# Optimization experiments

Hardware: AMD Instinct MI355X
Metric: run time of the kernel (lower is better)

Reference implementation:

```python
import jax, jax.numpy as jnp
import numpy as np

D_M = 1024
NUM_TOK = 4096


def setup_inputs() -> dict:
    key = jax.random.key(0)
    ks = jax.random.split(key, 7)
    mk = lambda k, shp: jax.random.normal(k, shp, dtype=jnp.float32) * 0.02
    return {
        "X": jax.random.normal(ks[0], (D_M, NUM_TOK), dtype=jnp.float32),
        "W_Q": mk(ks[1], (D_M, D_M)),
        "W_K": mk(ks[2], (D_M, D_M)),
        "W_V": mk(ks[3], (D_M, D_M)),
        "W_O": mk(ks[4], (D_M, D_M)),
        "mlp_in": mk(ks[5], (D_M, D_M)),
        "mlp_out": mk(ks[6], (D_M, D_M)),
    }


def reference(X, W_Q, W_K, W_V, W_O, mlp_in, mlp_out):
    # X: [d_m, num_tok]; module transposes to tokens-major [N, d]
    Xt = X.T  # [N, d]
    N = Xt.shape[0]
    Q = Xt @ W_Q  # [N, d]
    K = Xt @ W_K  # [N, d]
    scores = Q @ K.T  # [N, N] -- NOTE: no 1/sqrt(d) scaling, as in the original
    causal = jnp.tril(jnp.ones((N, N), dtype=bool))  # keep lower triangle incl. diag
    scores = jnp.where(causal, scores, -jnp.inf)
    A = jax.nn.softmax(scores, axis=-1)  # [N, N]
    # original applies W_V then W_O to X BEFORE the attention mix
    RH = (Xt @ W_V) @ W_O  # [N, d]
    Xt = Xt + A @ RH  # residual + attention
    h = jax.nn.relu(Xt @ mlp_in)  # [N, d] (hidden dim == d_m in original)
    Xt = Xt + h @ mlp_out  # residual + MLP
    return Xt.T  # back to [d_m, num_tok]
```

## Files before the change

kernel.cpp:

```cpp
#include <hip/hip_runtime.h>
#include <stdint.h>
#include <stddef.h>

using f16 = _Float16;
typedef __attribute__((ext_vector_type(8))) _Float16 f16x8;
typedef __attribute__((ext_vector_type(4))) float f32x4;

__device__ __forceinline__ void async_copy16(const f16* g, f16* l) {
    __builtin_amdgcn_global_load_lds(
        (const __attribute__((address_space(1))) void*)g,
        (__attribute__((address_space(3))) void*)l, 16, 0, 0);
}

__global__ __launch_bounds__(256)
void prep_all(const float* __restrict__ X, float* __restrict__ Xtf,
              f16* __restrict__ Xth,
              const float* __restrict__ w0, const float* __restrict__ w1,
              const float* __restrict__ w2, const float* __restrict__ w3,
              const float* __restrict__ w4, const float* __restrict__ w5,
              f16* o0, f16* o1, f16* o2, f16* o3, f16* o4, f16* o5,
              int D, int NT) {
    __shared__ float tile[32][33];
    const int tx = threadIdx.x & 31, ty = threadIdx.x >> 5;
    int b = blockIdx.x;
    if (b < 4096) {
        const int c0 = (b & 127) * 32, r0 = (b >> 7) * 32;
#pragma unroll
        for (int j = 0; j < 4; j++)
            tile[ty + j * 8][tx] = X[(size_t)(r0 + ty + j * 8) * NT + c0 + tx];
        __syncthreads();
#pragma unroll
        for (int j = 0; j < 4; j++) {
            float v = tile[tx][ty + j * 8];
            size_t idx = (size_t)(c0 + ty + j * 8) * D + r0 + tx;
            Xtf[idx] = v;
            Xth[idx] = (f16)v;
        }
        return;
    }
    b -= 4096;
    const int z = b >> 10, r = b & 1023;
    const float* in = z == 0 ? w0 : z == 1 ? w1 : z == 2 ? w2 : z == 3 ? w3 : z == 4 ? w4 : w5;
    f16* out = z == 0 ? o0 : z == 1 ? o1 : z == 2 ? o2 : z == 3 ? o3 : z == 4 ? o4 : o5;
    const int c0 = (r & 31) * 32, r0 = (r >> 5) * 32;
    if (z < 3) {
#pragma unroll
        for (int j = 0; j < 4; j++) {
            size_t idx = (size_t)(r0 + ty + j * 8) * D + c0 + tx;
            out[idx] = (f16)in[idx];
        }
    } else {
#pragma unroll
        for (int j = 0; j < 4; j++)
            tile[ty + j * 8][tx] = in[(size_t)(r0 + ty + j * 8) * D + c0 + tx];
        __syncthreads();
#pragma unroll
        for (int j = 0; j < 4; j++)
            out[(size_t)(c0 + ty + j * 8) * D + r0 + tx] = (f16)tile[tx][ty + j * 8];
    }
}

__global__ __launch_bounds__(256)
void softmax_rows(f16* __restrict__ A, int N) {
    const int row = blockIdx.x, len = row + 1;
    const int lim = ((row >> 7) + 1) << 7;
    f16* a = A + (size_t)row * N;
    __shared__ float red[256];
    const int t = threadIdx.x;

    float v[16];
    float mx = -1e30f;
#pragma unroll
    for (int j = 0; j < 2; j++) {
        const int c = (t + j * 256) * 8;
        if (c < len) {
            f16x8 x = *(const f16x8*)(a + c);
#pragma unroll
            for (int e = 0; e < 8; e++) {
                float f = (c + e < len) ? (float)x[e] : -1e30f;
                v[j * 8 + e] = f;
                mx = fmaxf(mx, f);
            }
        } else {
#pragma unroll
            for (int e = 0; e < 8; e++) v[j * 8 + e] = -1e30f;
        }
    }
    red[t] = mx; __syncthreads();
    for (int o = 128; o > 0; o >>= 1) { if (t < o) red[t] = fmaxf(red[t], red[t + o]); __syncthreads(); }
    mx = red[0]; __syncthreads();

    float sum = 0.f;
#pragma unroll
    for (int k = 0; k < 16; k++) {
        float e = (v[k] > -1e29f) ? __expf(v[k] - mx) : 0.0f;
        v[k] = e;
        sum += e;
    }
    red[t] = sum; __syncthreads();
    for (int o = 128; o > 0; o >>= 1) { if (t < o) red[t] += red[t + o]; __syncthreads(); }
    const float inv = 1.0f / red[0];
#pragma unroll
    for (int j = 0; j < 2; j++) {
        const int c = (t + j * 256) * 8;
        if (c < lim) {
            f16x8 o8;
#pragma unroll
            for (int e = 0; e < 8; e++) o8[e] = (f16)(v[j * 8 + e] * inv);
            *(f16x8*)(a + c) = o8;
        }
    }
}


__device__ __forceinline__ void body64db(
    f16* lds, const f16* __restrict__ A, const f16* __restrict__ B,
    f16* __restrict__ Ch, int m0, int n0, int N, int K, int lda) {
    const int t = threadIdx.x;
    const int lane = t & 63, wave = t >> 6;
    const int wm = (wave >> 1) * 32, wn = (wave & 1) * 32;
    const int lm = lane & 15, lq = lane >> 4;
    const int srow = t >> 2;
    const int gs = ((t & 3) ^ ((srow >> 1) & 3)) * 8;
    const int rs = (lq ^ ((lm >> 1) & 3)) * 8;

    auto stage = [&](f16* buf, int k0) {
#pragma unroll
        for (int r = 0; r < 4; r++)
            async_copy16(A + (size_t)(m0 + srow) * lda + k0 + r * 32 + gs,
                         buf + r * 2048 + t * 8);
#pragma unroll
        for (int r = 0; r < 4; r++)
            async_copy16(B + (size_t)(n0 + srow) * K + k0 + r * 32 + gs,
                         buf + 8192 + r * 2048 + t * 8);
    };

    f32x4 acc[2][2] = {};
    stage(lds, 0);
    __syncthreads();
    int cur = 0;
    for (int k0 = 0; k0 < K; k0 += 128) {
        f16* cb = lds + cur * 16384;
        if (k0 + 128 < K) stage(lds + (cur ^ 1) * 16384, k0 + 128);
#pragma unroll
        for (int kk = 0; kk < 4; kk++) {
            f16x8 af[2], bf[2];
#pragma unroll
            for (int i = 0; i < 2; i++)
                af[i] = *(const f16x8*)&cb[kk * 2048 + (wm + i * 16 + lm) * 32 + rs];
#pragma unroll
            for (int j = 0; j < 2; j++)
                bf[j] = *(const f16x8*)&cb[8192 + kk * 2048 + (wn + j * 16 + lm) * 32 + rs];
#pragma unroll
            for (int i = 0; i < 2; i++)
#pragma unroll
                for (int j = 0; j < 2; j++)
                    acc[i][j] = __builtin_amdgcn_mfma_f32_16x16x32_f16(
                        af[i], bf[j], acc[i][j], 0, 0, 0);
        }
        __syncthreads();
        cur ^= 1;
    }

#pragma unroll
    for (int i = 0; i < 2; i++) {
        const int row = m0 + wm + i * 16 + lq * 4;
#pragma unroll
        for (int j = 0; j < 2; j++) {
            const int col = n0 + wn + j * 16 + lm;
            f32x4 v = acc[i][j];
#pragma unroll
            for (int r = 0; r < 4; r++)
                Ch[(size_t)(row + r) * N + col] = (f16)v[r];
        }
    }
}

template <int BN, int MODE>
__device__ __forceinline__ void body128db(
    f16* lds, const f16* __restrict__ A, const f16* __restrict__ B,
    float* __restrict__ Cf, f16* __restrict__ Ch, const float* __restrict__ resid,
    int m0, int n0, int M, int N, int K, int lda, int Keff) {
    const int t = threadIdx.x;
    const int lane = t & 63, wave = t >> 6;
    constexpr int WN = BN / 2;
    constexpr int NJ = WN / 16;
    constexpr int ASZ = 128 * 64;
    constexpr int BSZ = BN * 64;
    constexpr int BUF = ASZ + BSZ;
    const int wm = (wave >> 1) * 64, wn = (wave & 1) * WN;
    const int lm = lane & 15, lq = lane >> 4;
    const int srow = t >> 2;
    const int gs = ((t & 3) ^ ((srow >> 1) & 3)) * 8;
    const int rs = (lq ^ ((lm >> 1) & 3)) * 8;

    auto stage = [&](f16* buf, int k0) {
#pragma unroll
        for (int r = 0; r < 4; r++)
            async_copy16(A + (size_t)(m0 + (r & 1) * 64 + srow) * lda + k0 + (r >> 1) * 32 + gs,
                         buf + r * 2048 + t * 8);
        if constexpr (BN == 128) {
#pragma unroll
            for (int r = 0; r < 4; r++)
                async_copy16(B + (size_t)(n0 + (r & 1) * 64 + srow) * K + k0 + (r >> 1) * 32 + gs,
                             buf + ASZ + r * 2048 + t * 8);
        } else {
#pragma unroll
            for (int r = 0; r < 2; r++)
                async_copy16(B + (size_t)(n0 + srow) * K + k0 + r * 32 + gs,
                             buf + ASZ + r * 2048 + t * 8);
        }
    };

    f32x4 acc[4][NJ] = {};
    stage(lds, 0);
    __syncthreads();
    int cur = 0;
    for (int k0 = 0; k0 < Keff; k0 += 64) {
        f16* cb = lds + cur * BUF;
        if (k0 + 64 < Keff) stage(lds + (cur ^ 1) * BUF, k0 + 64);
#pragma unroll
        for (int kk = 0; kk < 2; kk++) {
            f16x8 af[4], bf[NJ];
#pragma unroll
            for (int i = 0; i < 4; i++)
                af[i] = *(const f16x8*)&cb[kk * 4096 + (wm + i * 16 + lm) * 32 + rs];
#pragma unroll
            for (int j = 0; j < NJ; j++)
                bf[j] = *(const f16x8*)&cb[ASZ + kk * (BN * 32) + (wn + j * 16 + lm) * 32 + rs];
#pragma unroll
            for (int i = 0; i < 4; i++)
#pragma unroll
                for (int j = 0; j < NJ; j++)
                    acc[i][j] = __builtin_amdgcn_mfma_f32_16x16x32_f16(
                        af[i], bf[j], acc[i][j], 0, 0, 0);
        }
        __syncthreads();
        cur ^= 1;
    }

#pragma unroll
    for (int i = 0; i < 4; i++) {
        const int row = m0 + wm + i * 16 + lq * 4;
#pragma unroll
        for (int j = 0; j < NJ; j++) {
            const int col = n0 + wn + j * 16 + lm;
            f32x4 v = acc[i][j];
#pragma unroll
            for (int r = 0; r < 4; r++) {
                if (MODE == 0) {
                    Ch[(size_t)(row + r) * N + col] = (f16)v[r];
                } else if (MODE == 2) {
                    float o = v[r] + resid[(size_t)(row + r) * N + col];
                    Cf[(size_t)(row + r) * N + col] = o;
                    Ch[(size_t)(row + r) * N + col] = (f16)o;
                } else if (MODE == 3) {
                    Ch[(size_t)(row + r) * N + col] = (f16)fmaxf(v[r], 0.0f);
                } else {
                    float o = v[r] + resid[(size_t)(row + r) * N + col];
                    Cf[(size_t)col * M + (row + r)] = o;
                }
            }
        }
    }
}

__global__ __launch_bounds__(256, 2)
void tiny_pair(const f16* Wkh, const f16* Wqh, f16* GT,
               const f16* Wot, const f16* Wvh, f16* HT) {
    __shared__ alignas(16) f16 smem[32768];
    const int b = blockIdx.x;
    if (b < 256)
        body64db(smem, Wkh, Wqh, GT,
                 (b >> 4) * 64, (b & 15) * 64, 1024, 1024, 1024);
    else {
        const int r = b - 256;
        body64db(smem, Wot, Wvh, HT,
                 (r >> 4) * 64, (r & 15) * 64, 1024, 1024, 1024);
    }
}

__global__ __launch_bounds__(256, 2)
void mid_pair(const f16* Xth, const f16* GT, f16* Qp,
              const f16* HT, f16* RHt) {
    __shared__ alignas(16) f16 smem[32768];
    const int x = blockIdx.x & 7;
    int s = blockIdx.x >> 3;
    if (s < 32) {
        const int m = x + 8 * (s >> 3), n = s & 7;
        body128db<128, 0>(smem, Xth, GT, nullptr, Qp, nullptr,
                          m * 128, n * 128, 4096, 1024, 1024, 1024, 1024);
    } else {
        s -= 32;
        const int n = x + 8 * (s >> 3), m = s & 7;
        body128db<128, 0>(smem, HT, Xth, nullptr, RHt, nullptr,
                          m * 128, n * 128, 1024, 4096, 1024, 1024, 1024);
    }
}

__global__ __launch_bounds__(256, 2)
void scores_tri(const f16* Qp, const f16* Xth, f16* Af) {
    __shared__ alignas(16) f16 smem[32768];
    const int x = blockIdx.x & 7;
    int s = blockIdx.x >> 3;
    int m = 0, n = 0;
#pragma unroll
    for (int q = 3; q >= 0; q--) {
        const int mm = 8 * q + ((q & 1) ? 7 - x : x);
        if (s < mm + 1) { m = mm; n = s; break; }
        s -= mm + 1;
    }
    body128db<128, 0>(smem, Qp, Xth, nullptr, Af, nullptr,
                      m * 128, n * 128, 4096, 4096, 1024, 1024, 1024);
}

template <int MODE, bool CAUSAL_K>
__global__ __launch_bounds__(256, 2)
void gemm_n64(const f16* __restrict__ A, const f16* __restrict__ B,
              float* __restrict__ Cf, f16* __restrict__ Ch,
              const float* __restrict__ resid, int M, int N, int K, int lda) {
    __shared__ alignas(16) f16 smem[24576];
    const int x = blockIdx.x & 7, s = blockIdx.x >> 3;
    const int qs = s >> 4, n = s & 15;
    int m;
    if (CAUSAL_K) {
        const int q = (qs == 0) ? 3 : (qs == 1) ? 2 : (qs == 2) ? 0 : 1;
        m = 8 * q + ((q & 1) ? 7 - x : x);
    } else {
        m = x + 8 * qs;
    }
    const int m0 = m * 128, n0 = n * 64;
    int Keff = K;
    if (CAUSAL_K) {
        Keff = m0 + 128;
        if (Keff > K) Keff = K;
    }
    body128db<64, MODE>(smem, A, B, Cf, Ch, resid,
                        m0, n0, M, N, K, lda, Keff);
}

extern "C" void kernel_launch(void* const* d_in, const int* in_sizes, int n_in,
                              void* d_out, int out_size, void* d_ws, size_t ws_size,
                              hipStream_t stream) {
    const int D = 1024, NT = 4096;
    const float* X = (const float*)d_in[0];
    const float* W[6] = {(const float*)d_in[1], (const float*)d_in[2],
                         (const float*)d_in[3], (const float*)d_in[4],
                         (const float*)d_in[5], (const float*)d_in[6]};
    char* ws = (char*)d_ws;
    auto MB = [](size_t x) { return x << 20; };

    float* Xtf  = (float*)(ws + MB(0));
    f16*   Xth  = (f16*)(ws + MB(16));
    f16*   Wqh  = (f16*)(ws + MB(24));
    f16*   Wkh  = (f16*)(ws + MB(26));
    f16*   Wvh  = (f16*)(ws + MB(28));
    f16*   Wot  = (f16*)(ws + MB(30));
    f16*   W4t  = (f16*)(ws + MB(32));
    f16*   W5t  = (f16*)(ws + MB(34));
    f16*   GT   = (f16*)(ws + MB(36));
    f16*   HT   = (f16*)(ws + MB(38));
    f16*   Qp   = (f16*)(ws + MB(40));
    f16*   Af   = (f16*)(ws + MB(48));
    f16*   RHt  = (f16*)(ws + MB(80));
    float* Y1f  = (float*)(ws + MB(88));
    f16*   Y1h  = (f16*)(ws + MB(104));
    f16*   hb   = (f16*)(ws + MB(40));
    float* outF = (float*)d_out;

    prep_all<<<10240, 256, 0, stream>>>(X, Xtf, Xth, W[0], W[1], W[2], W[3],
                                        W[4], W[5], Wqh, Wkh, Wvh, Wot, W4t,
                                        W5t, D, NT);

    tiny_pair<<<512, 256, 0, stream>>>(Wkh, Wqh, GT, Wot, Wvh, HT);

    mid_pair<<<512, 256, 0, stream>>>(Xth, GT, Qp, HT, RHt);

    scores_tri<<<528, 256, 0, stream>>>(Qp, Xth, Af);

    softmax_rows<<<NT, 256, 0, stream>>>(Af, NT);

    gemm_n64<2, true><<<512, 256, 0, stream>>>(
        Af, RHt, Y1f, Y1h, Xtf, NT, D, NT, NT);

    gemm_n64<3, false><<<512, 256, 0, stream>>>(
        Y1h, W4t, nullptr, hb, nullptr, NT, D, D, D);

    gemm_n64<4, false><<<512, 256, 0, stream>>>(
        hb, W5t, outF, nullptr, Y1f, NT, D, D, D);
}
```

Baseline: 241.3 us.

## Use triple-buffered 128x64 GEMM with prefetch depth two and explicit vmcnt waits

Replaces the double-buffered 128xBN GEMM body with a three-stage LDS ring that keeps two k-tiles in flight, using explicit s_waitcnt vmcnt and raw s_barrier with sched_barrier fences instead of __syncthreads. The 128x128 tiles in mid_pair and scores_tri become 128x64 tiles, doubling grid sizes and changing the triangular tile mapping. The aim is to hide global-to-LDS latency and raise wave parallelism. The cost is more LDS per block, which may limit occupancy, and the hand-counted vmcnt values must match the number of outstanding loads per stage.

```diff
diff --git a/kernel.cpp b/kernel.cpp
--- a/kernel.cpp
+++ b/kernel.cpp
@@ -10,6 +10,13 @@
     __builtin_amdgcn_global_load_lds(
         (const __attribute__((address_space(1))) void*)g,
         (__attribute__((address_space(3))) void*)l, 16, 0, 0);
+}
+
+template <int N>
+__device__ __forceinline__ void wait_vmcnt() {
+    if constexpr (N == 0)       asm volatile("s_waitcnt vmcnt(0)" ::: "memory");
+    else if constexpr (N == 6)  asm volatile("s_waitcnt vmcnt(6)" ::: "memory");
+    else if constexpr (N == 12) asm volatile("s_waitcnt vmcnt(12)" ::: "memory");
 }
 
 __global__ __launch_bounds__(256)
@@ -113,137 +120,83 @@
 }
 
 
-__device__ __forceinline__ void body64db(
+template <int MODE>
+__device__ __forceinline__ void body_pf2(
     f16* lds, const f16* __restrict__ A, const f16* __restrict__ B,
-    f16* __restrict__ Ch, int m0, int n0, int N, int K, int lda) {
+    float* __restrict__ Cf, f16* __restrict__ Ch, const float* __restrict__ resid,
+    int m0, int n0, int M, int N, int K, int lda, int Keff) {
+    constexpr int ASZ = 128 * 64;
+    constexpr int BSZ = 64 * 64;
+    constexpr int SSZ = ASZ + BSZ;
     const int t = threadIdx.x;
     const int lane = t & 63, wave = t >> 6;
-    const int wm = (wave >> 1) * 32, wn = (wave & 1) * 32;
+    const int wm = (wave >> 1) * 64, wn = (wave & 1) * 32;
     const int lm = lane & 15, lq = lane >> 4;
     const int srow = t >> 2;
     const int gs = ((t & 3) ^ ((srow >> 1) & 3)) * 8;
     const int rs = (lq ^ ((lm >> 1) & 3)) * 8;
 
+    f32x4 acc[4][2] = {};
+
     auto stage = [&](f16* buf, int k0) {
 #pragma unroll
         for (int r = 0; r < 4; r++)
-            async_copy16(A + (size_t)(m0 + srow) * lda + k0 + r * 32 + gs,
+            async_copy16(A + (size_t)(m0 + (r & 1) * 64 + srow) * lda + k0 + (r >> 1) * 32 + gs,
                          buf + r * 2048 + t * 8);
 #pragma unroll
-        for (int r = 0; r < 4; r++)
+        for (int r = 0; r < 2; r++)
             async_copy16(B + (size_t)(n0 + srow) * K + k0 + r * 32 + gs,
-                         buf + 8192 + r * 2048 + t * 8);
+                         buf + ASZ + r * 2048 + t * 8);
     };
 
-    f32x4 acc[2][2] = {};
-    stage(lds, 0);
-    __syncthreads();
-    int cur = 0;
-    for (int k0 = 0; k0 < K; k0 += 128) {
-        f16* cb = lds + cur * 16384;
-        if (k0 + 128 < K) stage(lds + (cur ^ 1) * 16384, k0 + 128);
-#pragma unroll
-        for (int kk = 0; kk < 4; kk++) {
-            f16x8 af[2], bf[2];
-#pragma unroll
-            for (int i = 0; i < 2; i++)
-                af[i] = *(const f16x8*)&cb[kk * 2048 + (wm + i * 16 + lm) * 32 + rs];
+    auto compute = [&](const f16* cb) {
+#pragma unroll
+        for (int kk = 0; kk < 2; kk++) {
+            f16x8 af[4], bf[2];
+#pragma unroll
+            for (int i = 0; i < 4; i++)
+                af[i] = *(const f16x8*)&cb[kk * 4096 + (wm + i * 16 + lm) * 32 + rs];
 #pragma unroll
             for (int j = 0; j < 2; j++)
-                bf[j] = *(const f16x8*)&cb[8192 + kk * 2048 + (wn + j * 16 + lm) * 32 + rs];
-#pragma unroll
-            for (int i = 0; i < 2; i++)
+                bf[j] = *(const f16x8*)&cb[ASZ + kk * 2048 + (wn + j * 16 + lm) * 32 + rs];
+#pragma unroll
+            for (int i = 0; i < 4; i++)
 #pragma unroll
                 for (int j = 0; j < 2; j++)
                     acc[i][j] = __builtin_amdgcn_mfma_f32_16x16x32_f16(
                         af[i], bf[j], acc[i][j], 0, 0, 0);
         }
-        __syncthreads();
-        cur ^= 1;
-    }
-
-#pragma unroll
-    for (int i = 0; i < 2; i++) {
-        const int row = m0 + wm + i * 16 + lq * 4;
-#pragma unroll
-        for (int j = 0; j < 2; j++) {
-            const int col = n0 + wn + j * 16 + lm;
-            f32x4 v = acc[i][j];
-#pragma unroll
-            for (int r = 0; r < 4; r++)
-                Ch[(size_t)(row + r) * N + col] = (f16)v[r];
-        }
-    }
-}
-
-template <int BN, int MODE>
-__device__ __forceinline__ void body128db(
-    f16* lds, const f16* __restrict__ A, const f16* __restrict__ B,
-    float* __restrict__ Cf, f16* __restrict__ Ch, const float* __restrict__ resid,
-    int m0, int n0, int M, int N, int K, int lda, int Keff) {
-    const int t = threadIdx.x;
-    const int lane = t & 63, wave = t >> 6;
-    constexpr int WN = BN / 2;
-    constexpr int NJ = WN / 16;
-    constexpr int ASZ = 128 * 64;
-    constexpr int BSZ = BN * 64;
-    constexpr int BUF = ASZ + BSZ;
-    const int wm = (wave >> 1) * 64, wn = (wave & 1) * WN;
-    const int lm = lane & 15, lq = lane >> 4;
-    const int srow = t >> 2;
-    const int gs = ((t & 3) ^ ((srow >> 1) & 3)) * 8;
-    const int rs = (lq ^ ((lm >> 1) & 3)) * 8;
-
-    auto stage = [&](f16* buf, int k0) {
-#pragma unroll
-        for (int r = 0; r < 4; r++)
-            async_copy16(A + (size_t)(m0 + (r & 1) * 64 + srow) * lda + k0 + (r >> 1) * 32 + gs,
-                         buf + r * 2048 + t * 8);
-        if constexpr (BN == 128) {
-#pragma unroll
-            for (int r = 0; r < 4; r++)
-                async_copy16(B + (size_t)(n0 + (r & 1) * 64 + srow) * K + k0 + (r >> 1) * 32 + gs,
-                             buf + ASZ + r * 2048 + t * 8);
+    };
+
+    f16 *pa = lds, *pb = lds + SSZ, *pc = lds + 2 * SSZ;
+    stage(pa, 0);
+    stage(pb, 64);
+    const int NS = Keff >> 6;
+    for (int s = 0; s < NS; s++) {
+        const int k2 = (s + 2) << 6;
+        if (k2 < Keff) {
+            stage(pc, k2);
+            wait_vmcnt<12>();
+        } else if (s + 1 < NS) {
+            wait_vmcnt<6>();
         } else {
-#pragma unroll
-            for (int r = 0; r < 2; r++)
-                async_copy16(B + (size_t)(n0 + srow) * K + k0 + r * 32 + gs,
-                             buf + ASZ + r * 2048 + t * 8);
-        }
-    };
-
-    f32x4 acc[4][NJ] = {};
-    stage(lds, 0);
-    __syncthreads();
-    int cur = 0;
-    for (int k0 = 0; k0 < Keff; k0 += 64) {
-        f16* cb = lds + cur * BUF;
-        if (k0 + 64 < Keff) stage(lds + (cur ^ 1) * BUF, k0 + 64);
-#pragma unroll
-        for (int kk = 0; kk < 2; kk++) {
-            f16x8 af[4], bf[NJ];
-#pragma unroll
-            for (int i = 0; i < 4; i++)
-                af[i] = *(const f16x8*)&cb[kk * 4096 + (wm + i * 16 + lm) * 32 + rs];
-#pragma unroll
-            for (int j = 0; j < NJ; j++)
-                bf[j] = *(const f16x8*)&cb[ASZ + kk * (BN * 32) + (wn + j * 16 + lm) * 32 + rs];
-#pragma unroll
-            for (int i = 0; i < 4; i++)
-#pragma unroll
-                for (int j = 0; j < NJ; j++)
-                    acc[i][j] = __builtin_amdgcn_mfma_f32_16x16x32_f16(
-                        af[i], bf[j], acc[i][j], 0, 0, 0);
-        }
-        __syncthreads();
-        cur ^= 1;
+            wait_vmcnt<0>();
+        }
+        __builtin_amdgcn_sched_barrier(0);
+        __builtin_amdgcn_s_barrier();
+        __builtin_amdgcn_sched_barrier(0);
+        compute(pa);
+        __builtin_amdgcn_sched_barrier(0);
+        __builtin_amdgcn_s_barrier();
+        __builtin_amdgcn_sched_barrier(0);
+        f16* tp = pa; pa = pb; pb = pc; pc = tp;
     }
 
 #pragma unroll
     for (int i = 0; i < 4; i++) {
         const int row = m0 + wm + i * 16 + lq * 4;
 #pragma unroll
-        for (int j = 0; j < NJ; j++) {
+        for (int j = 0; j < 2; j++) {
             const int col = n0 + wn + j * 16 + lm;
             f32x4 v = acc[i][j];
 #pragma unroll
@@ -265,6 +218,69 @@
     }
 }
 
+__device__ __forceinline__ void body64db(
+    f16* lds, const f16* __restrict__ A, const f16* __restrict__ B,
+    f16* __restrict__ Ch, int m0, int n0, int N, int K, int lda) {
+    const int t = threadIdx.x;
+    const int lane = t & 63, wave = t >> 6;
+    const int wm = (wave >> 1) * 32, wn = (wave & 1) * 32;
+    const int lm = lane & 15, lq = lane >> 4;
+    const int srow = t >> 2;
+    const int gs = ((t & 3) ^ ((srow >> 1) & 3)) * 8;
+    const int rs = (lq ^ ((lm >> 1) & 3)) * 8;
+
+    auto stage = [&](f16* buf, int k0) {
+#pragma unroll
+        for (int r = 0; r < 4; r++)
+            async_copy16(A + (size_t)(m0 + srow) * lda + k0 + r * 32 + gs,
+                         buf + r * 2048 + t * 8);
+#pragma unroll
+        for (int r = 0; r < 4; r++)
+            async_copy16(B + (size_t)(n0 + srow) * K + k0 + r * 32 + gs,
+                         buf + 8192 + r * 2048 + t * 8);
+    };
+
+    f32x4 acc[2][2] = {};
+    stage(lds, 0);
+    __syncthreads();
+    int cur = 0;
+    for (int k0 = 0; k0 < K; k0 += 128) {
+        f16* cb = lds + cur * 16384;
+        if (k0 + 128 < K) stage(lds + (cur ^ 1) * 16384, k0 + 128);
+#pragma unroll
+        for (int kk = 0; kk < 4; kk++) {
+            f16x8 af[2], bf[2];
+#pragma unroll
+            for (int i = 0; i < 2; i++)
+                af[i] = *(const f16x8*)&cb[kk * 2048 + (wm + i * 16 + lm) * 32 + rs];
+#pragma unroll
+            for (int j = 0; j < 2; j++)
+                bf[j] = *(const f16x8*)&cb[8192 + kk * 2048 + (wn + j * 16 + lm) * 32 + rs];
+#pragma unroll
+            for (int i = 0; i < 2; i++)
+#pragma unroll
+                for (int j = 0; j < 2; j++)
+                    acc[i][j] = __builtin_amdgcn_mfma_f32_16x16x32_f16(
+                        af[i], bf[j], acc[i][j], 0, 0, 0);
+        }
+        __syncthreads();
+        cur ^= 1;
+    }
+
+#pragma unroll
+    for (int i = 0; i < 2; i++) {
+        const int row = m0 + wm + i * 16 + lq * 4;
+#pragma unroll
+        for (int j = 0; j < 2; j++) {
+            const int col = n0 + wn + j * 16 + lm;
+            f32x4 v = acc[i][j];
+#pragma unroll
+            for (int r = 0; r < 4; r++)
+                Ch[(size_t)(row + r) * N + col] = (f16)v[r];
+        }
+    }
+}
+
 __global__ __launch_bounds__(256, 2)
 void tiny_pair(const f16* Wkh, const f16* Wqh, f16* GT,
                const f16* Wot, const f16* Wvh, f16* HT) {
@@ -283,43 +299,44 @@
 __global__ __launch_bounds__(256, 2)
 void mid_pair(const f16* Xth, const f16* GT, f16* Qp,
               const f16* HT, f16* RHt) {
-    __shared__ alignas(16) f16 smem[32768];
+    __shared__ alignas(16) f16 smem[36864];
     const int x = blockIdx.x & 7;
     int s = blockIdx.x >> 3;
-    if (s < 32) {
-        const int m = x + 8 * (s >> 3), n = s & 7;
-        body128db<128, 0>(smem, Xth, GT, nullptr, Qp, nullptr,
-                          m * 128, n * 128, 4096, 1024, 1024, 1024, 1024);
+    if (s < 64) {
+        const int m = x + 8 * (s >> 4), n = s & 15;
+        body_pf2<0>(smem, Xth, GT, nullptr, Qp, nullptr,
+                    m * 128, n * 64, 4096, 1024, 1024, 1024, 1024);
     } else {
-        s -= 32;
+        s -= 64;
         const int n = x + 8 * (s >> 3), m = s & 7;
-        body128db<128, 0>(smem, HT, Xth, nullptr, RHt, nullptr,
-                          m * 128, n * 128, 1024, 4096, 1024, 1024, 1024);
+        body_pf2<0>(smem, HT, Xth, nullptr, RHt, nullptr,
+                    m * 128, n * 64, 1024, 4096, 1024, 1024, 1024);
     }
 }
 
 __global__ __launch_bounds__(256, 2)
 void scores_tri(const f16* Qp, const f16* Xth, f16* Af) {
-    __shared__ alignas(16) f16 smem[32768];
+    __shared__ alignas(16) f16 smem[36864];
     const int x = blockIdx.x & 7;
     int s = blockIdx.x >> 3;
+    const int cand[4] = {31 - x, 16 + x, 15 - x, x};
     int m = 0, n = 0;
 #pragma unroll
-    for (int q = 3; q >= 0; q--) {
-        const int mm = 8 * q + ((q & 1) ? 7 - x : x);
-        if (s < mm + 1) { m = mm; n = s; break; }
-        s -= mm + 1;
-    }
-    body128db<128, 0>(smem, Qp, Xth, nullptr, Af, nullptr,
-                      m * 128, n * 128, 4096, 4096, 1024, 1024, 1024);
+    for (int i = 0; i < 4; i++) {
+        const int c = 2 * cand[i] + 2;
+        if (s < c) { m = cand[i]; n = s; break; }
+        s -= c;
+    }
+    body_pf2<0>(smem, Qp, Xth, nullptr, Af, nullptr,
+                m * 128, n * 64, 4096, 4096, 1024, 1024, 1024);
 }
 
 template <int MODE, bool CAUSAL_K>
 __global__ __launch_bounds__(256, 2)
-void gemm_n64(const f16* __restrict__ A, const f16* __restrict__ B,
+void gemm_nar(const f16* __restrict__ A, const f16* __restrict__ B,
               float* __restrict__ Cf, f16* __restrict__ Ch,
               const float* __restrict__ resid, int M, int N, int K, int lda) {
-    __shared__ alignas(16) f16 smem[24576];
+    __shared__ alignas(16) f16 smem[36864];
     const int x = blockIdx.x & 7, s = blockIdx.x >> 3;
     const int qs = s >> 4, n = s & 15;
     int m;
@@ -335,8 +352,8 @@
         Keff = m0 + 128;
         if (Keff > K) Keff = K;
     }
-    body128db<64, MODE>(smem, A, B, Cf, Ch, resid,
-                        m0, n0, M, N, K, lda, Keff);
+    body_pf2<MODE>(smem, A, B, Cf, Ch, resid,
+                   m0, n0, M, N, K, lda, Keff);
 }
 
 extern "C" void kernel_launch(void* const* d_in, const int* in_sizes, int n_in,
@@ -374,18 +391,18 @@
 
     tiny_pair<<<512, 256, 0, stream>>>(Wkh, Wqh, GT, Wot, Wvh, HT);
 
-    mid_pair<<<512, 256, 0, stream>>>(Xth, GT, Qp, HT, RHt);
-
-    scores_tri<<<528, 256, 0, stream>>>(Qp, Xth, Af);
+    mid_pair<<<1024, 256, 0, stream>>>(Xth, GT, Qp, HT, RHt);
+
+    scores_tri<<<1056, 256, 0, stream>>>(Qp, Xth, Af);
 
     softmax_rows<<<NT, 256, 0, stream>>>(Af, NT);
 
-    gemm_n64<2, true><<<512, 256, 0, stream>>>(
+    gemm_nar<2, true><<<512, 256, 0, stream>>>(
         Af, RHt, Y1f, Y1h, Xtf, NT, D, NT, NT);
 
-    gemm_n64<3, false><<<512, 256, 0, stream>>>(
+    gemm_nar<3, false><<<512, 256, 0, stream>>>(
         Y1h, W4t, nullptr, hb, nullptr, NT, D, D, D);
 
-    gemm_n64<4, false><<<512, 256, 0, stream>>>(
+    gemm_nar<4, false><<<512, 256, 0, stream>>>(
         hb, W5t, outF, nullptr, Y1f, NT, D, D, D);
 }
```

New measurement: 235.7 us. 1.02x faster.
